# Optimization experiments

Hardware: AMD Instinct MI355X
Metric: run time of the kernel (lower is better)

The kernel has to match this reference:

```python
import jax, jax.numpy as jnp
import numpy as np

B, M_IN, N_OUT = 131072, 64, 64


def setup_inputs() -> dict:
    key = jax.random.key(0)
    k1, k2, k3 = jax.random.split(key, 3)
    x = jax.random.normal(k1, (B, M_IN, 4), dtype=jnp.float32)
    x = x.at[:, :, 0].set(0.0)  # pure quaternion input (w-component = 0)
    stdv_w = (2.0 / (M_IN + N_OUT)) ** 0.5
    W_q = jax.random.normal(k2, (N_OUT, M_IN, 4), dtype=jnp.float32) * (stdv_w / 2.0)
    theta_q = jax.random.normal(k3, (N_OUT, 4), dtype=jnp.float32) * 0.01
    theta_q = theta_q.at[:, 0].set(0.0)  # pure quaternion threshold
    return {"x_batch": x, "W_q": W_q, "theta_q": theta_q}


def _hamilton_sum(x, W):
    """s[b,n] = sum_m W[n,m] (x) x[b,m]  (Hamilton product, W on the left).
    x: (B, M, 4), W: (N, M, 4) -> (B, N, 4)"""
    ww, wx, wy, wz = (W[..., i] for i in range(4))   # each (N, M)
    xw, xx, xy, xz = (x[..., i] for i in range(4))   # each (B, M)
    dot = lambda p, q: jnp.einsum('bm,nm->bn', p, q)
    sw = dot(xw, ww) - dot(xx, wx) - dot(xy, wy) - dot(xz, wz)
    sx = dot(xx, ww) + dot(xw, wx) + dot(xz, wy) - dot(xy, wz)
    sy = dot(xy, ww) - dot(xz, wx) + dot(xw, wy) + dot(xx, wz)
    sz = dot(xz, ww) + dot(xy, wx) - dot(xx, wy) + dot(xw, wz)
    return jnp.stack([sw, sx, sy, sz], axis=-1)


def reference(x_batch, W_q, theta_q):
    # Isokawa quaternion neuron: s = sum_m W (x) x - theta; y = sigmoid(s) per component.
    s = _hamilton_sum(x_batch, W_q) - theta_q[None, :, :]  # (B, N, 4) pre-activation (s_internal)
    return jax.nn.sigmoid(s)
```

## Files before the change

kernel.cpp:

```cpp
#include <hip/hip_runtime.h>
#include <hip/hip_bf16.h>


typedef __bf16 bf16_t;
typedef bf16_t bf16x8 __attribute__((ext_vector_type(8)));
typedef bf16_t bf16x4v __attribute__((ext_vector_type(4)));
typedef float f32x4 __attribute__((ext_vector_type(4)));

#define B_TOTAL 131072
#define KDIM 256
#define NDIM 256
#define ROWS 64
#define THREADS 512
#define LDS_STRIDE 264

__global__ void coef_kernel(const float* __restrict__ W, bf16_t* __restrict__ coef) {
    const int widx[4][4] = {{0,1,2,3},{1,0,3,2},{2,3,0,1},{3,2,1,0}};
    const float sgn[4][4] = {{1.f,-1.f,-1.f,-1.f},
                             {1.f, 1.f,-1.f, 1.f},
                             {1.f, 1.f, 1.f,-1.f},
                             {1.f,-1.f, 1.f, 1.f}};
    int F = blockIdx.x * blockDim.x + threadIdx.x;
    int j    = F & 7;
    int lane = (F >> 3) & 63;
    int ks   = (F >> 9) & 7;
    int nt   = F >> 12;
    int col  = nt * 16 + (lane & 15);
    int k    = ks * 32 + (lane >> 4) * 8 + j;
    int n = col >> 2, oc = col & 3;
    int m = k >> 2,   ic = k & 3;
    coef[F] = (bf16_t)(sgn[oc][ic] * W[n * 256 + m * 4 + widx[oc][ic]]);
}

__global__ __launch_bounds__(THREADS, 4)
void main_kernel(const float* __restrict__ x, const bf16x8* __restrict__ coef,
                 const float* __restrict__ theta, float* __restrict__ out) {
    __shared__ __align__(16) bf16_t xs[ROWS * LDS_STRIDE];

    const int tid  = threadIdx.x;
    const int row0 = blockIdx.x * ROWS;
    const int wave = tid >> 6, lane = tid & 63;
    const int l15  = lane & 15, quad = lane >> 4;

    const float4* xp = (const float4*)(x + (long)row0 * KDIM);
    float4 v[8];
#pragma unroll
    for (int i = 0; i < 8; i++) v[i] = xp[tid + THREADS * i];

    bf16x8 breg[2][8];
#pragma unroll
    for (int ct = 0; ct < 2; ct++)
#pragma unroll
        for (int ks = 0; ks < 8; ks++)
            breg[ct][ks] = coef[((wave * 2 + ct) * 8 + ks) * 64 + lane];

#pragma unroll
    for (int i = 0; i < 8; i++) {
        int f = tid + THREADS * i;
        int r = f >> 6;
        int c = (f & 63) * 4;
        bf16x4v w;
        w.x = (bf16_t)v[i].x; w.y = (bf16_t)v[i].y;
        w.z = (bf16_t)v[i].z; w.w = (bf16_t)v[i].w;
        *(bf16x4v*)&xs[r * LDS_STRIDE + c] = w;
    }
    __syncthreads();

    f32x4 acc[4][2];
#pragma unroll
    for (int rt = 0; rt < 4; rt++)
#pragma unroll
        for (int ct = 0; ct < 2; ct++) acc[rt][ct] = (f32x4)(0.f);

#pragma unroll
    for (int ks = 0; ks < 8; ks++) {
        bf16x8 a[4];
#pragma unroll
        for (int rt = 0; rt < 4; rt++)
            a[rt] = *(const bf16x8*)&xs[(rt * 16 + l15) * LDS_STRIDE + ks * 32 + quad * 8];
#pragma unroll
        for (int rt = 0; rt < 4; rt++)
#pragma unroll
            for (int ct = 0; ct < 2; ct++)
                acc[rt][ct] = __builtin_amdgcn_mfma_f32_16x16x32_bf16(
                    a[rt], breg[ct][ks], acc[rt][ct], 0, 0, 0);
    }

    float th[2];
#pragma unroll
    for (int ct = 0; ct < 2; ct++) th[ct] = theta[wave * 32 + ct * 16 + l15];

#pragma unroll
    for (int rt = 0; rt < 4; rt++) {
        int rbase = row0 + rt * 16 + quad * 4;
#pragma unroll
        for (int ct = 0; ct < 2; ct++) {
            int col = wave * 32 + ct * 16 + l15;
#pragma unroll
            for (int r = 0; r < 4; r++) {
                float s = acc[rt][ct][r] - th[ct];
                float y = 1.0f / (1.0f + __expf(-s));
                out[(long)(rbase + r) * NDIM + col] = y;
            }
        }
    }
}

extern "C" void kernel_launch(void* const* d_in, const int* in_sizes, int n_in,
                              void* d_out, int out_size, void* d_ws, size_t ws_size,
                              hipStream_t stream) {
    const float* x     = (const float*)d_in[0];
    const float* W     = (const float*)d_in[1];
    const float* theta = (const float*)d_in[2];
    float* out = (float*)d_out;
    bf16_t* coef = (bf16_t*)d_ws;

    if (ws_size < 65536 * sizeof(bf16_t)) return;

    coef_kernel<<<256, 256, 0, stream>>>(W, coef);
    main_kernel<<<B_TOTAL / ROWS, THREADS, 0, stream>>>(
        x, (const bf16x8*)coef, theta, out);
}
```

Measured before the change: 242.9 us.

## Persistent grid with register-prefetched x tiles and column-split waves

Replaces the one-block-per-64-rows launch with a fixed 512-block persistent grid. Each block owns one half of the output columns and loops over 8 row tiles, prefetching the next tile of x into registers while the current one is computed. The MFMA operands are swapped so each lane holds 4 consecutive output columns, which allows float4 output stores, and the sigmoid uses a fast reciprocal. The trade-off is that every x row is now loaded and converted twice, once per column half, and the smaller grid may not fill the GPU as well.

```diff
diff --git a/kernel.cpp b/kernel.cpp
--- a/kernel.cpp
+++ b/kernel.cpp
@@ -12,6 +12,8 @@
 #define NDIM 256
 #define ROWS 64
 #define THREADS 512
+#define GRID 512
+#define TILES 8
 #define LDS_STRIDE 264
 
 __global__ void coef_kernel(const float* __restrict__ W, bf16_t* __restrict__ coef) {
@@ -32,76 +34,80 @@
     coef[F] = (bf16_t)(sgn[oc][ic] * W[n * 256 + m * 4 + widx[oc][ic]]);
 }
 
+__device__ __forceinline__ void wg_barrier() {
+    asm volatile("s_waitcnt lgkmcnt(0)\n\ts_barrier" ::: "memory");
+}
+
 __global__ __launch_bounds__(THREADS, 4)
 void main_kernel(const float* __restrict__ x, const bf16x8* __restrict__ coef,
                  const float* __restrict__ theta, float* __restrict__ out) {
     __shared__ __align__(16) bf16_t xs[ROWS * LDS_STRIDE];
 
     const int tid  = threadIdx.x;
-    const int row0 = blockIdx.x * ROWS;
+    const int bid  = blockIdx.x;
     const int wave = tid >> 6, lane = tid & 63;
     const int l15  = lane & 15, quad = lane >> 4;
+    const int colhalf = bid >> 8;
+    const int rowblk  = bid & 255;
+    const int nt   = colhalf * 8 + wave;
+    const int col0 = nt * 16 + quad * 4;
 
-    const float4* xp = (const float4*)(x + (long)row0 * KDIM);
+    const float4* xp = (const float4*)(x + (size_t)rowblk * ROWS * KDIM);
     float4 v[8];
 #pragma unroll
     for (int i = 0; i < 8; i++) v[i] = xp[tid + THREADS * i];
 
-    bf16x8 breg[2][8];
+    bf16x8 breg[8];
 #pragma unroll
-    for (int ct = 0; ct < 2; ct++)
+    for (int ks = 0; ks < 8; ks++)
+        breg[ks] = coef[(nt * 8 + ks) * 64 + lane];
+
+    const float4 th = *(const float4*)&theta[col0];
+
+    for (int t = 0; t < TILES; t++) {
+        const size_t row0 = (size_t)(rowblk + 256 * t) * ROWS;
+
+        wg_barrier();
+#pragma unroll
+        for (int i = 0; i < 8; i++) {
+            int f = tid + THREADS * i;
+            int r = f >> 6;
+            int c = (f & 63) * 4;
+            bf16x4v w;
+            w.x = (bf16_t)v[i].x; w.y = (bf16_t)v[i].y;
+            w.z = (bf16_t)v[i].z; w.w = (bf16_t)v[i].w;
+            *(bf16x4v*)&xs[r * LDS_STRIDE + c] = w;
+        }
+        if (t + 1 < TILES) {
+            const float4* xn = (const float4*)(x + (size_t)(rowblk + 256 * (t + 1)) * ROWS * KDIM);
+#pragma unroll
+            for (int i = 0; i < 8; i++) v[i] = xn[tid + THREADS * i];
+        }
+        wg_barrier();
+
+        f32x4 acc[4];
+#pragma unroll
+        for (int rt = 0; rt < 4; rt++) acc[rt] = (f32x4)(0.f);
+
 #pragma unroll
         for (int ks = 0; ks < 8; ks++)
-            breg[ct][ks] = coef[((wave * 2 + ct) * 8 + ks) * 64 + lane];
+#pragma unroll
+            for (int rt = 0; rt < 4; rt++) {
+                bf16x8 xf = *(const bf16x8*)
+                    &xs[(rt * 16 + l15) * LDS_STRIDE + ks * 32 + quad * 8];
+                acc[rt] = __builtin_amdgcn_mfma_f32_16x16x32_bf16(
+                    breg[ks], xf, acc[rt], 0, 0, 0);
+            }
 
 #pragma unroll
-    for (int i = 0; i < 8; i++) {
-        int f = tid + THREADS * i;
-        int r = f >> 6;
-        int c = (f & 63) * 4;
-        bf16x4v w;
-        w.x = (bf16_t)v[i].x; w.y = (bf16_t)v[i].y;
-        w.z = (bf16_t)v[i].z; w.w = (bf16_t)v[i].w;
-        *(bf16x4v*)&xs[r * LDS_STRIDE + c] = w;
-    }
-    __syncthreads();
-
-    f32x4 acc[4][2];
-#pragma unroll
-    for (int rt = 0; rt < 4; rt++)
-#pragma unroll
-        for (int ct = 0; ct < 2; ct++) acc[rt][ct] = (f32x4)(0.f);
-
-#pragma unroll
-    for (int ks = 0; ks < 8; ks++) {
-        bf16x8 a[4];
-#pragma unroll
-        for (int rt = 0; rt < 4; rt++)
-            a[rt] = *(const bf16x8*)&xs[(rt * 16 + l15) * LDS_STRIDE + ks * 32 + quad * 8];
-#pragma unroll
-        for (int rt = 0; rt < 4; rt++)
-#pragma unroll
-            for (int ct = 0; ct < 2; ct++)
-                acc[rt][ct] = __builtin_amdgcn_mfma_f32_16x16x32_bf16(
-                    a[rt], breg[ct][ks], acc[rt][ct], 0, 0, 0);
-    }
-
-    float th[2];
-#pragma unroll
-    for (int ct = 0; ct < 2; ct++) th[ct] = theta[wave * 32 + ct * 16 + l15];
-
-#pragma unroll
-    for (int rt = 0; rt < 4; rt++) {
-        int rbase = row0 + rt * 16 + quad * 4;
-#pragma unroll
-        for (int ct = 0; ct < 2; ct++) {
-            int col = wave * 32 + ct * 16 + l15;
-#pragma unroll
-            for (int r = 0; r < 4; r++) {
-                float s = acc[rt][ct][r] - th[ct];
-                float y = 1.0f / (1.0f + __expf(-s));
-                out[(long)(rbase + r) * NDIM + col] = y;
-            }
+        for (int rt = 0; rt < 4; rt++) {
+            size_t row = row0 + rt * 16 + l15;
+            float4 y;
+            y.x = __builtin_amdgcn_rcpf(1.f + __expf(-(acc[rt][0] - th.x)));
+            y.y = __builtin_amdgcn_rcpf(1.f + __expf(-(acc[rt][1] - th.y)));
+            y.z = __builtin_amdgcn_rcpf(1.f + __expf(-(acc[rt][2] - th.z)));
+            y.w = __builtin_amdgcn_rcpf(1.f + __expf(-(acc[rt][3] - th.w)));
+            *(float4*)&out[row * NDIM + col0] = y;
         }
     }
 }
@@ -118,6 +124,6 @@
     if (ws_size < 65536 * sizeof(bf16_t)) return;
 
     coef_kernel<<<256, 256, 0, stream>>>(W, coef);
-    main_kernel<<<B_TOTAL / ROWS, THREADS, 0, stream>>>(
+    main_kernel<<<GRID, THREADS, 0, stream>>>(
         x, (const bf16x8*)coef, theta, out);
 }
```

New measurement: 252.5 us. 4.0% more time.
